# Kernel tuning notes

Measured on AMD Instinct MI355X. Metric: run time of the kernel, lower is better.

The kernel has to match this reference:

```python
import jax, jax.numpy as jnp
import numpy as np

H = 16          # num_heads
D = 64          # head_dim
EPS = 1e-6


def setup_inputs() -> dict:
    key = jax.random.key(0)
    ks = jax.random.split(key, 4)
    B, N, C = 4, 2048, 1024
    x = jax.random.normal(ks[0], (B, N, C), dtype=jnp.float32)
    w_qkv = jax.random.normal(ks[1], (C, 3 * C), dtype=jnp.float32) * (1.0 / np.sqrt(C))
    b_qkv = jnp.zeros((3 * C,), dtype=jnp.float32)
    g_q = jnp.ones((D,), dtype=jnp.float32)
    g_k = jnp.ones((D,), dtype=jnp.float32)
    w_proj = jax.random.normal(ks[2], (C, C), dtype=jnp.float32) * (1.0 / np.sqrt(C))
    b_proj = jnp.zeros((C,), dtype=jnp.float32)
    return {"x": x, "w_qkv": w_qkv, "b_qkv": b_qkv, "g_q": g_q, "g_k": g_k,
            "w_proj": w_proj, "b_proj": b_proj}


def _head_layernorm(t, gamma):
    # LayerNorm over last (head_dim) axis, no bias, with scale. t: [B,H,N,D]
    mu = jnp.mean(t, axis=-1, keepdims=True)
    var = jnp.mean(jnp.square(t - mu), axis=-1, keepdims=True)
    return (t - mu) * jax.lax.rsqrt(var + EPS) * gamma


def reference(x, w_qkv, b_qkv, g_q, g_k, w_proj, b_proj):
    B, N, C = x.shape
    qkv = x @ w_qkv + b_qkv                      # [B, N, 3C]
    qkv = qkv.reshape(B, N, 3, H, D)
    qkv = jnp.transpose(qkv, (2, 0, 3, 1, 4))    # [3, B, H, N, D]
    q, k, v = qkv[0], qkv[1], qkv[2]
    q = _head_layernorm(q, g_q)
    k = _head_layernorm(k, g_k)
    scale = D ** -0.5
    attn = jax.nn.softmax(jnp.einsum('bhqd,bhkd->bhqk', q, k) * scale, axis=-1)
    o = jnp.einsum('bhqk,bhkd->bhqd', attn, v)   # [B, H, N, D]
    o = o.transpose(0, 2, 1, 3).reshape(B, N, C)
    return o @ w_proj + b_proj
```

## Files before the change

kernel.cpp:

```cpp
#include <hip/hip_runtime.h>

#define HH 16
#define DD 64
#define BBATCH 4
#define NSEQ 2048
#define CDIM 1024
#define EPSLN 1e-6f

typedef __bf16 bf16x8 __attribute__((ext_vector_type(8)));
typedef float f32x4 __attribute__((ext_vector_type(4)));
typedef short s16x4 __attribute__((ext_vector_type(4)));
typedef short s16x8 __attribute__((ext_vector_type(8)));
typedef unsigned short u16;

__device__ inline u16 f2b(float f) {
  unsigned u = __builtin_bit_cast(unsigned, f);
  u += 0x7fffu + ((u >> 16) & 1u);
  return (u16)(u >> 16);
}
#if __has_builtin(__builtin_amdgcn_perm)
__device__ inline unsigned pack2(float a, float b) {
  unsigned ua = __builtin_bit_cast(unsigned, a) + 0x8000u;
  unsigned ub = __builtin_bit_cast(unsigned, b) + 0x8000u;
  return __builtin_amdgcn_perm(ub, ua, 0x07060302u);
}
#else
__device__ inline unsigned pack2(float a, float b) {
  unsigned ua = __builtin_bit_cast(unsigned, a);
  unsigned ub = __builtin_bit_cast(unsigned, b);
  return ((ua + 0x8000u) >> 16) | ((ub + 0x8000u) & 0xffff0000u);
}
#endif
#if __has_builtin(__builtin_amdgcn_exp2f)
#define EXP2(x) __builtin_amdgcn_exp2f(x)
#else
#define EXP2(x) __expf((x)*0.6931471805599453f)
#endif

__device__ inline bf16x8 ld_frag16(const u16* p) {
  s16x8 v = *(const s16x8*)p;
  return __builtin_bit_cast(bf16x8, v);
}
__device__ inline f32x4 mfma16(bf16x8 a, bf16x8 b, f32x4 c) {
  return __builtin_amdgcn_mfma_f32_16x16x32_bf16(a, b, c, 0, 0, 0);
}
__device__ inline void async16(const u16* g, u16* l) {
  __builtin_amdgcn_global_load_lds(
      (const __attribute__((address_space(1))) void*)g,
      (__attribute__((address_space(3))) void*)l, 16, 0, 0);
}

__global__ void cvt_x(const float* __restrict__ x, u16* __restrict__ xb) {
  long i = ((long)blockIdx.x * 256 + threadIdx.x) * 8;
  float4 a = *(const float4*)(x + i);
  float4 b = *(const float4*)(x + i + 4);
  u16 r[8];
  r[0] = f2b(a.x); r[1] = f2b(a.y); r[2] = f2b(a.z); r[3] = f2b(a.w);
  r[4] = f2b(b.x); r[5] = f2b(b.y); r[6] = f2b(b.z); r[7] = f2b(b.w);
  *(s16x8*)(xb + i) = *(s16x8*)r;
}

__global__ void cvt_wT(const float* __restrict__ w, u16* __restrict__ wT, int K, int N) {
  __shared__ float tile[32][33];
  int nt = N / 32;
  int bn = blockIdx.x % nt, bk = blockIdx.x / nt;
  int tx = threadIdx.x % 32, ty = threadIdx.x / 32;
  int k0 = bk * 32, n0 = bn * 32;
  for (int j = 0; j < 4; j++)
    tile[ty + 8 * j][tx] = w[(long)(k0 + ty + 8 * j) * N + n0 + tx];
  __syncthreads();
  for (int j = 0; j < 4; j++)
    wT[(long)(n0 + ty + 8 * j) * K + k0 + tx] = f2b(tile[tx][ty + 8 * j]);
}

__launch_bounds__(256, 3)
__global__ void gemm_qkv(const u16* __restrict__ A, const u16* __restrict__ BT,
                         const float* __restrict__ bias,
                         const float* __restrict__ gq, const float* __restrict__ gk,
                         u16* __restrict__ qb, u16* __restrict__ kb, u16* __restrict__ vtb) {
  const int Kd = CDIM;
  __shared__ u16 As[128 * 64];
  __shared__ u16 Bs[128 * 64];
  int t = threadIdx.x;
  int lane = t & 63, wave = t >> 6;
  int ln = lane & 15, quad = lane >> 4;
  int bm = blockIdx.x % 64, bn = blockIdx.x / 64;
  int wm = (wave >> 1) * 64, wn = (wave & 1) * 64;
  int r8 = t >> 3;
  int cb = (t & 7) * 8;
  int cg = (((t & 7) ^ (r8 & 7)) * 8);
  int swl = ln & 7;
  const u16* aB = A + (long)(bm * 128) * Kd + cg;
  const u16* bB = BT + (long)(bn * 128) * Kd + cg;
  f32x4 acc[4][4] = {};
  for (int kt = 0; kt < Kd / 64; kt++) {
    __syncthreads();
#pragma unroll
    for (int c = 0; c < 4; c++) {
      int row = c * 32 + r8;
      async16(aB + (long)row * Kd + kt * 64, As + row * 64 + cb);
      async16(bB + (long)row * Kd + kt * 64, Bs + row * 64 + cb);
    }
    __syncthreads();
#pragma unroll
    for (int kk = 0; kk < 2; kk++) {
      bf16x8 af[4], bfv[4];
#pragma unroll
      for (int mt = 0; mt < 4; mt++)
        af[mt] = ld_frag16(As + (wm + mt * 16 + ln) * 64 + (((kk * 4 + quad) ^ swl) * 8));
#pragma unroll
      for (int nt = 0; nt < 4; nt++)
        bfv[nt] = ld_frag16(Bs + (wn + nt * 16 + ln) * 64 + (((kk * 4 + quad) ^ swl) * 8));
#pragma unroll
      for (int mt = 0; mt < 4; mt++)
#pragma unroll
        for (int nt = 0; nt < 4; nt++)
          acc[mt][nt] = mfma16(af[mt], bfv[nt], acc[mt][nt]);
    }
  }
  int tq = bn >> 3;
  int colbase = bn * 128 + wn;
  int h = (colbase >> 6) & 15;
  int mbase = bm * 128 + wm;
  float bv[4];
#pragma unroll
  for (int nt = 0; nt < 4; nt++) bv[nt] = bias[colbase + nt * 16 + ln];
  if (tq == 2) {
#pragma unroll
    for (int mt = 0; mt < 4; mt++) {
      int m0 = mbase + mt * 16 + quad * 4;
      int b = m0 >> 11, n0 = m0 & 2047;
#pragma unroll
      for (int nt = 0; nt < 4; nt++) {
        int d = nt * 16 + ln;
        u16 pk[4];
#pragma unroll
        for (int r = 0; r < 4; r++) pk[r] = f2b(acc[mt][nt][r] + bv[nt]);
        *(s16x4*)(vtb + ((long)((b * HH + h) * DD + d)) * NSEQ + n0) = *(s16x4*)pk;
      }
    }
  } else {
    const float* g = (tq == 0) ? gq : gk;
    float extra = (tq == 0) ? 0.125f * 1.4426950408889634f : 1.0f;
    u16* dst = (tq == 0) ? qb : kb;
    float gv[4];
#pragma unroll
    for (int nt = 0; nt < 4; nt++) gv[nt] = g[nt * 16 + ln] * extra;
#pragma unroll
    for (int mt = 0; mt < 4; mt++)
#pragma unroll
      for (int r = 0; r < 4; r++) {
        float vv[4];
        float s1 = 0.f, s2 = 0.f;
#pragma unroll
        for (int nt = 0; nt < 4; nt++) {
          vv[nt] = acc[mt][nt][r] + bv[nt];
          s1 += vv[nt];
          s2 += vv[nt] * vv[nt];
        }
#pragma unroll
        for (int m = 1; m < 16; m <<= 1) {
          s1 += __shfl_xor(s1, m);
          s2 += __shfl_xor(s2, m);
        }
        float mu = s1 * (1.0f / 64.0f);
        float var = s2 * (1.0f / 64.0f) - mu * mu;
        float rstd = rsqrtf(var + EPSLN);
        int m = mbase + mt * 16 + quad * 4 + r;
        int b = m >> 11, n = m & 2047;
        long base = ((long)((b * HH + h) * NSEQ + n)) * DD;
#pragma unroll
        for (int nt = 0; nt < 4; nt++)
          dst[base + nt * 16 + ln] = f2b((vv[nt] - mu) * rstd * gv[nt]);
      }
  }
}

#define ATTN_TILE_COMPUTE()                                                      \
  _Pragma("unroll")                                                              \
  for (int qt = 0; qt < 4; qt++) {                                               \
    _Pragma("unroll")                                                            \
    for (int ctl = 0; ctl < 2; ctl++) {                                          \
      int ct = qt * 2 + ctl;                                                     \
      const u16* ka = Ks + (ct * 16 + ln) * 64;                                  \
      bf16x8 k0 = ld_frag16(ka + ((quad ^ swl) * 8));                            \
      bf16x8 k1 = ld_frag16(ka + (((quad + 4) ^ swl) * 8));                      \
      int poffc = (ctl * 16 + quad * 4) ^ psw;                                   \
      _Pragma("unroll")                                                          \
      for (int qf = 0; qf < 2; qf++) {                                           \
        f32x4 z = {};                                                            \
        z = mfma16(k0, bq[qf][0], z);                                            \
        z = mfma16(k1, bq[qf][1], z);                                            \
        float e0 = EXP2(z[0]), e1 = EXP2(z[1]), e2 = EXP2(z[2]), e3 = EXP2(z[3]);\
        rs[qf] += (e0 + e1) + (e2 + e3);                                         \
        uint2 pk;                                                                \
        pk.x = pack2(e0, e1);                                                    \
        pk.y = pack2(e2, e3);                                                    \
        *(uint2*)(Pw + (qf * 16 + ln) * 32 + poffc) = pk;                        \
      }                                                                          \
    }                                                                            \
    bf16x8 pA[2];                                                                \
    _Pragma("unroll")                                                            \
    for (int qf = 0; qf < 2; qf++)                                               \
      pA[qf] = ld_frag16(Pw + (qf * 16 + ln) * 32 + ((quad * 8) ^ psw));         \
    _Pragma("unroll")                                                            \
    for (int dt = 0; dt < 4; dt++) {                                             \
      const u16* vrow = Vs + (dt * 16 + ln) * 128;                               \
      bf16x8 vv = ld_frag16(vrow + (((4 * qt + quad) ^ swl) * 8));               \
      __builtin_amdgcn_s_setprio(1);                                             \
      _Pragma("unroll")                                                          \
      for (int qf = 0; qf < 2; qf++)                                             \
        o[qf][dt] = mfma16(pA[qf], vv, o[qf][dt]);                               \
      __builtin_amdgcn_s_setprio(0);                                             \
    }                                                                            \
  }

__launch_bounds__(256, 4)
__global__ void attn(const u16* __restrict__ qb, const u16* __restrict__ kb,
                     const u16* __restrict__ vtb, u16* __restrict__ ob) {
  __shared__ u16 smem[20480];
  u16* Ks = smem;
  u16* Vs = smem + 8192;
  u16* Pl = smem + 16384;
  int t = threadIdx.x, lane = t & 63, wave = t >> 6;
  int ln = lane & 15, quad = lane >> 4;
  int g = blockIdx.x;
  int bh = (g & 7) * 8 + ((g >> 3) & 7);
  int qblk = g >> 6;
  int b = bh >> 4, h = bh & 15;
  const u16* qg = qb + (long)bh * NSEQ * DD;
  const u16* kg = kb + (long)bh * NSEQ * DD;
  const u16* vg = vtb + (long)bh * DD * NSEQ;
  int qrow0 = qblk * 128 + wave * 32;
  bf16x8 bq[2][2];
#pragma unroll
  for (int qf = 0; qf < 2; qf++)
#pragma unroll
    for (int kk = 0; kk < 2; kk++)
      bq[qf][kk] = ld_frag16(qg + (long)(qrow0 + qf * 16 + ln) * DD + kk * 32 + quad * 8);
  f32x4 o[2][4] = {};
  float rs[2] = {0.f, 0.f};
  u16* Pw = Pl + wave * 1024;
  int psw = (ln & 3) * 8;
  int swl = ln & 7;
  int cK = (lane & 7) ^ (lane >> 3);
  int rV = lane >> 4;

  int lr3 = lane >> 3;
  const u16* kpfB = kg + (long)(wave * 8 + lr3) * DD + cK * 8;
  int cV = (lane & 15) ^ ((wave * 4 + rV) & 7);
  const u16* vpfB = vg + (long)(wave * 4 + rV) * NSEQ + cV * 8;
  u16* kdst = Ks + wave * 8 * 64 + lane * 8;
  u16* vdst = Vs + wave * 4 * 128 + lane * 8;

#pragma unroll
  for (int c = 0; c < 4; c++) {
    int rowb = c * 32 + wave * 8;
    async16(kg + (long)(rowb + lr3) * DD + cK * 8, Ks + rowb * 64 + lane * 8);
  }
#pragma unroll
  for (int c = 0; c < 4; c++) {
    int drow = c * 16 + wave * 4;
    int rv = drow + rV;
    async16(vg + (long)rv * NSEQ + cV * 8, Vs + drow * 128 + lane * 8);
  }
  __syncthreads();

  for (int kv = 0; kv < NSEQ / 128 - 1; kv++) {
    const u16* ks = kpfB + (long)(kv + 1) * 128 * DD;
    const u16* vs = vpfB + (long)(kv + 1) * 128;
    uint4 ka0 = *(const uint4*)(ks);
    uint4 ka1 = *(const uint4*)(ks + 32 * DD);
    uint4 ka2 = *(const uint4*)(ks + 64 * DD);
    uint4 ka3 = *(const uint4*)(ks + 96 * DD);
    uint4 va0 = *(const uint4*)(vs);
    uint4 va1 = *(const uint4*)(vs + (long)16 * NSEQ);
    uint4 va2 = *(const uint4*)(vs + (long)32 * NSEQ);
    uint4 va3 = *(const uint4*)(vs + (long)48 * NSEQ);
    __builtin_amdgcn_sched_barrier(0);
    ATTN_TILE_COMPUTE();
    __syncthreads();
    *(uint4*)(kdst) = ka0;
    *(uint4*)(kdst + 32 * 64) = ka1;
    *(uint4*)(kdst + 64 * 64) = ka2;
    *(uint4*)(kdst + 96 * 64) = ka3;
    *(uint4*)(vdst) = va0;
    *(uint4*)(vdst + 16 * 128) = va1;
    *(uint4*)(vdst + 32 * 128) = va2;
    *(uint4*)(vdst + 48 * 128) = va3;
    __syncthreads();
  }
  ATTN_TILE_COMPUTE();

#pragma unroll
  for (int qf = 0; qf < 2; qf++) {
    float r2 = rs[qf];
    r2 += __shfl_xor(r2, 16);
    r2 += __shfl_xor(r2, 32);
#pragma unroll
    for (int r = 0; r < 4; r++) {
      float inv = 1.0f / __shfl(r2, quad * 4 + r);
      int n = qrow0 + qf * 16 + quad * 4 + r;
      long base = ((long)(b * NSEQ + n) * HH + h) * DD;
#pragma unroll
      for (int dt = 0; dt < 4; dt++)
        ob[base + dt * 16 + ln] = f2b(o[qf][dt][r] * inv);
    }
  }
}

__launch_bounds__(256, 3)
__global__ void gemm_proj(const u16* __restrict__ A, const u16* __restrict__ BT,
                          const float* __restrict__ bias, float* __restrict__ out) {
  const int Kd = CDIM;
  __shared__ u16 As[128 * 64];
  __shared__ u16 Bs[128 * 64];
  int t = threadIdx.x;
  int lane = t & 63, wave = t >> 6;
  int ln = lane & 15, quad = lane >> 4;
  int bm = blockIdx.x % 64, bn = blockIdx.x / 64;
  int wm = (wave >> 1) * 64, wn = (wave & 1) * 64;
  int r8 = t >> 3;
  int cb = (t & 7) * 8;
  int cg = (((t & 7) ^ (r8 & 7)) * 8);
  int swl = ln & 7;
  const u16* aB = A + (long)(bm * 128) * Kd + cg;
  const u16* bB = BT + (long)(bn * 128) * Kd + cg;
  f32x4 acc[4][4] = {};
  for (int kt = 0; kt < Kd / 64; kt++) {
    __syncthreads();
#pragma unroll
    for (int c = 0; c < 4; c++) {
      int row = c * 32 + r8;
      async16(aB + (long)row * Kd + kt * 64, As + row * 64 + cb);
      async16(bB + (long)row * Kd + kt * 64, Bs + row * 64 + cb);
    }
    __syncthreads();
#pragma unroll
    for (int kk = 0; kk < 2; kk++) {
      bf16x8 af[4], bfv[4];
#pragma unroll
      for (int mt = 0; mt < 4; mt++)
        af[mt] = ld_frag16(As + (wm + mt * 16 + ln) * 64 + (((kk * 4 + quad) ^ swl) * 8));
#pragma unroll
      for (int nt = 0; nt < 4; nt++)
        bfv[nt] = ld_frag16(Bs + (wn + nt * 16 + ln) * 64 + (((kk * 4 + quad) ^ swl) * 8));
#pragma unroll
      for (int mt = 0; mt < 4; mt++)
#pragma unroll
        for (int nt = 0; nt < 4; nt++)
          acc[mt][nt] = mfma16(af[mt], bfv[nt], acc[mt][nt]);
    }
  }
#pragma unroll
  for (int mt = 0; mt < 4; mt++)
#pragma unroll
    for (int nt = 0; nt < 4; nt++) {
      int col = bn * 128 + wn + nt * 16 + ln;
      float bvx = bias[col];
#pragma unroll
      for (int r = 0; r < 4; r++) {
        int m = bm * 128 + wm + mt * 16 + quad * 4 + r;
        out[(long)m * CDIM + col] = acc[mt][nt][r] + bvx;
      }
    }
}

extern "C" void kernel_launch(void* const* d_in, const int* in_sizes, int n_in,
                              void* d_out, int out_size, void* d_ws, size_t ws_size,
                              hipStream_t stream) {
  const float* x = (const float*)d_in[0];
  const float* w_qkv = (const float*)d_in[1];
  const float* b_qkv = (const float*)d_in[2];
  const float* g_q = (const float*)d_in[3];
  const float* g_k = (const float*)d_in[4];
  const float* w_proj = (const float*)d_in[5];
  const float* b_proj = (const float*)d_in[6];
  float* out = (float*)d_out;

  char* ws = (char*)d_ws;
  const size_t MB = 1024 * 1024;
  u16* xb = (u16*)ws;
  u16* wqkvT = (u16*)(ws + 16 * MB);
  u16* wprojT = (u16*)(ws + 22 * MB);
  u16* qb = (u16*)(ws + 24 * MB);
  u16* kb = (u16*)(ws + 40 * MB);
  u16* vtb = (u16*)(ws + 56 * MB);
  u16* ob = xb;

  cvt_x<<<4096, 256, 0, stream>>>(x, xb);
  cvt_wT<<<(1024 / 32) * (3072 / 32), 256, 0, stream>>>(w_qkv, wqkvT, CDIM, 3 * CDIM);
  cvt_wT<<<(1024 / 32) * (1024 / 32), 256, 0, stream>>>(w_proj, wprojT, CDIM, CDIM);
  gemm_qkv<<<64 * 24, 256, 0, stream>>>(xb, wqkvT, b_qkv, g_q, g_k, qb, kb, vtb);
  attn<<<1024, 256, 0, stream>>>(qb, kb, vtb, ob);
  gemm_proj<<<64 * 8, 256, 0, stream>>>(ob, wprojT, b_proj, out);
}
```

Baseline: 290.6 us.

## Switch attention to 32x32x16 MFMA with register-resident P via lane shuffles

Rewrites the attention inner tile to use 32x32x16 bf16 MFMAs, with each wave covering 64 query rows instead of 32. The S^T tile is transposed into the P operand layout through cross-half-wave shuffles rather than a round trip through LDS, so the per-wave P scratch buffer is removed. The grid is halved to 512 blocks with launch bounds of 2 blocks per CU, raising register use per thread and doubling K/V reuse per block. Output stores are widened to 4-element packed writes. The cost is lower occupancy and only 512 blocks to spread across the CUs, which risks under-utilisation and tail effects.

```diff
diff --git a/kernel.cpp b/kernel.cpp
--- a/kernel.cpp
+++ b/kernel.cpp
@@ -9,6 +9,7 @@
 
 typedef __bf16 bf16x8 __attribute__((ext_vector_type(8)));
 typedef float f32x4 __attribute__((ext_vector_type(4)));
+typedef float f32x16 __attribute__((ext_vector_type(16)));
 typedef short s16x4 __attribute__((ext_vector_type(4)));
 typedef short s16x8 __attribute__((ext_vector_type(8)));
 typedef unsigned short u16;
@@ -43,6 +44,9 @@
 }
 __device__ inline f32x4 mfma16(bf16x8 a, bf16x8 b, f32x4 c) {
   return __builtin_amdgcn_mfma_f32_16x16x32_bf16(a, b, c, 0, 0, 0);
+}
+__device__ inline f32x16 mfma32(bf16x8 a, bf16x8 b, f32x16 c) {
+  return __builtin_amdgcn_mfma_f32_32x32x16_bf16(a, b, c, 0, 0, 0);
 }
 __device__ inline void async16(const u16* g, u16* l) {
   __builtin_amdgcn_global_load_lds(
@@ -176,73 +180,86 @@
   }
 }
 
-#define ATTN_TILE_COMPUTE()                                                      \
-  _Pragma("unroll")                                                              \
-  for (int qt = 0; qt < 4; qt++) {                                               \
-    _Pragma("unroll")                                                            \
-    for (int ctl = 0; ctl < 2; ctl++) {                                          \
-      int ct = qt * 2 + ctl;                                                     \
-      const u16* ka = Ks + (ct * 16 + ln) * 64;                                  \
-      bf16x8 k0 = ld_frag16(ka + ((quad ^ swl) * 8));                            \
-      bf16x8 k1 = ld_frag16(ka + (((quad + 4) ^ swl) * 8));                      \
-      int poffc = (ctl * 16 + quad * 4) ^ psw;                                   \
-      _Pragma("unroll")                                                          \
-      for (int qf = 0; qf < 2; qf++) {                                           \
-        f32x4 z = {};                                                            \
-        z = mfma16(k0, bq[qf][0], z);                                            \
-        z = mfma16(k1, bq[qf][1], z);                                            \
-        float e0 = EXP2(z[0]), e1 = EXP2(z[1]), e2 = EXP2(z[2]), e3 = EXP2(z[3]);\
-        rs[qf] += (e0 + e1) + (e2 + e3);                                         \
-        uint2 pk;                                                                \
-        pk.x = pack2(e0, e1);                                                    \
-        pk.y = pack2(e2, e3);                                                    \
-        *(uint2*)(Pw + (qf * 16 + ln) * 32 + poffc) = pk;                        \
-      }                                                                          \
-    }                                                                            \
-    bf16x8 pA[2];                                                                \
-    _Pragma("unroll")                                                            \
-    for (int qf = 0; qf < 2; qf++)                                               \
-      pA[qf] = ld_frag16(Pw + (qf * 16 + ln) * 32 + ((quad * 8) ^ psw));         \
-    _Pragma("unroll")                                                            \
-    for (int dt = 0; dt < 4; dt++) {                                             \
-      const u16* vrow = Vs + (dt * 16 + ln) * 128;                               \
-      bf16x8 vv = ld_frag16(vrow + (((4 * qt + quad) ^ swl) * 8));               \
-      __builtin_amdgcn_s_setprio(1);                                             \
-      _Pragma("unroll")                                                          \
-      for (int qf = 0; qf < 2; qf++)                                             \
-        o[qf][dt] = mfma16(pA[qf], vv, o[qf][dt]);                               \
-      __builtin_amdgcn_s_setprio(0);                                             \
-    }                                                                            \
-  }
-
-__launch_bounds__(256, 4)
-__global__ void attn(const u16* __restrict__ qb, const u16* __restrict__ kb,
+#define ATTN_TILE_COMPUTE()                                                       \
+  _Pragma("unroll")                                                               \
+  for (int kbq = 0; kbq < 4; kbq++) {                                             \
+    const u16* kaB = Ks + (kbq * 32 + l) * 64;                                    \
+    bf16x8 ak0 = ld_frag16(kaB + (((0 + hl) ^ sw3) * 8));                         \
+    bf16x8 ak1 = ld_frag16(kaB + (((2 + hl) ^ sw3) * 8));                         \
+    bf16x8 ak2 = ld_frag16(kaB + (((4 + hl) ^ sw3) * 8));                         \
+    bf16x8 ak3 = ld_frag16(kaB + (((6 + hl) ^ sw3) * 8));                         \
+    const u16* vaB = Vs + l * 128;                                                \
+    bf16x8 av00 = ld_frag16(vaB + (((kbq * 4 + 0 + hl) ^ sw3) * 8));              \
+    bf16x8 av01 = ld_frag16(vaB + (((kbq * 4 + 2 + hl) ^ sw3) * 8));              \
+    bf16x8 av10 = ld_frag16(vaB + 32 * 128 + (((kbq * 4 + 0 + hl) ^ sw3) * 8));   \
+    bf16x8 av11 = ld_frag16(vaB + 32 * 128 + (((kbq * 4 + 2 + hl) ^ sw3) * 8));   \
+    _Pragma("unroll")                                                             \
+    for (int qc = 0; qc < 2; qc++) {                                              \
+      f32x16 z = {};                                                              \
+      z = mfma32(ak0, bq[qc][0], z);                                              \
+      z = mfma32(ak1, bq[qc][1], z);                                              \
+      z = mfma32(ak2, bq[qc][2], z);                                              \
+      z = mfma32(ak3, bq[qc][3], z);                                              \
+      float e0 = EXP2(z[0]), e1 = EXP2(z[1]), e2 = EXP2(z[2]), e3 = EXP2(z[3]);   \
+      float e4 = EXP2(z[4]), e5 = EXP2(z[5]), e6 = EXP2(z[6]), e7 = EXP2(z[7]);   \
+      float e8 = EXP2(z[8]), e9 = EXP2(z[9]), e10 = EXP2(z[10]), e11 = EXP2(z[11]);\
+      float e12 = EXP2(z[12]), e13 = EXP2(z[13]), e14 = EXP2(z[14]), e15 = EXP2(z[15]);\
+      rs[qc] += (((e0 + e1) + (e2 + e3)) + ((e4 + e5) + (e6 + e7))) +             \
+                (((e8 + e9) + (e10 + e11)) + ((e12 + e13) + (e14 + e15)));        \
+      unsigned A0 = pack2(e0, e1), A1 = pack2(e2, e3);                            \
+      unsigned B0 = pack2(e4, e5), B1 = pack2(e6, e7);                            \
+      unsigned C0 = pack2(e8, e9), C1 = pack2(e10, e11);                          \
+      unsigned D0 = pack2(e12, e13), D1 = pack2(e14, e15);                        \
+      unsigned xA0 = __shfl_xor(A0, 32), xA1 = __shfl_xor(A1, 32);                \
+      unsigned xB0 = __shfl_xor(B0, 32), xB1 = __shfl_xor(B1, 32);                \
+      unsigned xC0 = __shfl_xor(C0, 32), xC1 = __shfl_xor(C1, 32);                \
+      unsigned xD0 = __shfl_xor(D0, 32), xD1 = __shfl_xor(D1, 32);                \
+      uint4 wa;                                                                   \
+      wa.x = hl ? xB0 : A0;                                                       \
+      wa.y = hl ? xB1 : A1;                                                       \
+      wa.z = hl ? B0 : xA0;                                                       \
+      wa.w = hl ? B1 : xA1;                                                       \
+      bf16x8 pb0 = __builtin_bit_cast(bf16x8, wa);                                \
+      uint4 wb;                                                                   \
+      wb.x = hl ? xD0 : C0;                                                       \
+      wb.y = hl ? xD1 : C1;                                                       \
+      wb.z = hl ? D0 : xC0;                                                       \
+      wb.w = hl ? D1 : xC1;                                                       \
+      bf16x8 pb1 = __builtin_bit_cast(bf16x8, wb);                                \
+      __builtin_amdgcn_s_setprio(1);                                              \
+      o[0][qc] = mfma32(av00, pb0, o[0][qc]);                                     \
+      o[0][qc] = mfma32(av01, pb1, o[0][qc]);                                     \
+      o[1][qc] = mfma32(av10, pb0, o[1][qc]);                                     \
+      o[1][qc] = mfma32(av11, pb1, o[1][qc]);                                     \
+      __builtin_amdgcn_s_setprio(0);                                              \
+    }                                                                             \
+  }
+
+__launch_bounds__(256, 2)
+__global__ void attn(const u16* __restrict__ qb, const u16* __restrict__ kbuf,
                      const u16* __restrict__ vtb, u16* __restrict__ ob) {
-  __shared__ u16 smem[20480];
+  __shared__ u16 smem[16384];
   u16* Ks = smem;
   u16* Vs = smem + 8192;
-  u16* Pl = smem + 16384;
   int t = threadIdx.x, lane = t & 63, wave = t >> 6;
-  int ln = lane & 15, quad = lane >> 4;
+  int l = lane & 31, hl = lane >> 5;
+  int sw3 = l & 7;
   int g = blockIdx.x;
   int bh = (g & 7) * 8 + ((g >> 3) & 7);
-  int qblk = g >> 6;
-  int b = bh >> 4, h = bh & 15;
+  int qblk = (g >> 6) & 7;
+  int b = bh >> 4, hh = bh & 15;
   const u16* qg = qb + (long)bh * NSEQ * DD;
-  const u16* kg = kb + (long)bh * NSEQ * DD;
+  const u16* kg = kbuf + (long)bh * NSEQ * DD;
   const u16* vg = vtb + (long)bh * DD * NSEQ;
-  int qrow0 = qblk * 128 + wave * 32;
-  bf16x8 bq[2][2];
-#pragma unroll
-  for (int qf = 0; qf < 2; qf++)
-#pragma unroll
-    for (int kk = 0; kk < 2; kk++)
-      bq[qf][kk] = ld_frag16(qg + (long)(qrow0 + qf * 16 + ln) * DD + kk * 32 + quad * 8);
-  f32x4 o[2][4] = {};
+  int qrow0 = qblk * 256 + wave * 64;
+  bf16x8 bq[2][4];
+#pragma unroll
+  for (int qc = 0; qc < 2; qc++)
+#pragma unroll
+    for (int ds = 0; ds < 4; ds++)
+      bq[qc][ds] = ld_frag16(qg + (long)(qrow0 + qc * 32 + l) * DD + ds * 16 + hl * 8);
+  f32x16 o[2][2] = {};
   float rs[2] = {0.f, 0.f};
-  u16* Pw = Pl + wave * 1024;
-  int psw = (ln & 3) * 8;
-  int swl = ln & 7;
   int cK = (lane & 7) ^ (lane >> 3);
   int rV = lane >> 4;
 
@@ -293,19 +310,20 @@
   ATTN_TILE_COMPUTE();
 
 #pragma unroll
-  for (int qf = 0; qf < 2; qf++) {
-    float r2 = rs[qf];
-    r2 += __shfl_xor(r2, 16);
-    r2 += __shfl_xor(r2, 32);
-#pragma unroll
-    for (int r = 0; r < 4; r++) {
-      float inv = 1.0f / __shfl(r2, quad * 4 + r);
-      int n = qrow0 + qf * 16 + quad * 4 + r;
-      long base = ((long)(b * NSEQ + n) * HH + h) * DD;
-#pragma unroll
-      for (int dt = 0; dt < 4; dt++)
-        ob[base + dt * 16 + ln] = f2b(o[qf][dt][r] * inv);
-    }
+  for (int qc = 0; qc < 2; qc++) {
+    float r2 = rs[qc] + __shfl_xor(rs[qc], 32);
+    float inv = 1.0f / r2;
+    int n = qrow0 + qc * 32 + l;
+    long base = ((long)(b * NSEQ + n) * HH + hh) * DD;
+#pragma unroll
+    for (int db = 0; db < 2; db++)
+#pragma unroll
+      for (int rq = 0; rq < 4; rq++) {
+        u16 pk[4];
+#pragma unroll
+        for (int j = 0; j < 4; j++) pk[j] = f2b(o[db][qc][rq * 4 + j] * inv);
+        *(s16x4*)(ob + base + db * 32 + rq * 8 + hl * 4) = *(s16x4*)pk;
+      }
   }
 }
 
@@ -392,6 +410,6 @@
   cvt_wT<<<(1024 / 32) * (3072 / 32), 256, 0, stream>>>(w_qkv, wqkvT, CDIM, 3 * CDIM);
   cvt_wT<<<(1024 / 32) * (1024 / 32), 256, 0, stream>>>(w_proj, wprojT, CDIM, CDIM);
   gemm_qkv<<<64 * 24, 256, 0, stream>>>(xb, wqkvT, b_qkv, g_q, g_k, qb, kb, vtb);
-  attn<<<1024, 256, 0, stream>>>(qb, kb, vtb, ob);
+  attn<<<512, 256, 0, stream>>>(qb, kb, vtb, ob);
   gemm_proj<<<64 * 8, 256, 0, stream>>>(ob, wprojT, b_proj, out);
 }
```

Measured after the change: 262.0 us. -9.8%, faster.
